# Kernel tuning notes

Hardware: AMD Instinct MI355X
Metric: run time of the kernel (lower is better)

The kernel has to match this reference:

```python
import jax, jax.numpy as jnp
import numpy as np

B, L, V, E, D, OUT = 64, 256, 50000, 512, 512, 3
PAD_IDX = 0
MAX_DIST = 11
NEG_INF = -1e9


def _mlp2(x, W1, b1, W2, b2):
    # Linear -> ReLU -> (Dropout=id) -> Linear -> ReLU -> (Dropout=id)
    h = jax.nn.relu(x @ W1 + b1)
    return jax.nn.relu(h @ W2 + b2)


def _masked_softmax(x, mask):
    return jax.nn.softmax(jnp.where(mask, x, NEG_INF), axis=-1)


def _rel_bias(n, dist_W):
    pos = jnp.arange(n)
    idx = jnp.clip(pos[None, :] - pos[:, None], -MAX_DIST, MAX_DIST) + MAX_DIST
    return dist_W[idx, 0]  # [n, n]


def _self_branch(x, mask, dist_W, Ws1, bs1, Ws2, bs2):
    # DeepDotAttention(x, x): shared MLP then dot scores [B, L, L]
    q = _mlp2(x, Ws1, bs1, Ws2, bs2)
    scores = jnp.einsum('bqd,bkd->bqk', q, q)
    n = x.shape[1]
    scores = scores + _rel_bias(n, dist_W)[None]           # relative-distance bias
    scores = jnp.where(jnp.eye(n, dtype=bool)[None], -jnp.inf, scores)  # mask diagonal
    scores = jnp.where(mask[:, None, :], scores, 0.0)      # zero padded keys (pre-softmax, as original)
    att = _masked_softmax(scores, mask[:, None, :])
    ctx = jnp.einsum('bqk,bkd->bqd', att, x)
    return jnp.concatenate([x, ctx], axis=-1)               # [B, L, 2E]


def setup_inputs() -> dict:
    key = jax.random.key(0)
    ks = jax.random.split(key, 20)

    def xavier(k, shape):
        fan_in, fan_out = shape[0], shape[1]
        lim = float(np.sqrt(6.0 / (fan_in + fan_out)))
        return jax.random.uniform(k, shape, jnp.float32, -lim, lim)

    embed_W = jax.random.normal(ks[0], (V, E), jnp.float32) * 0.1
    embed_W = embed_W.at[PAD_IDX].set(0.0)  # padding_idx
    inp = {
        'prem_input': jax.random.randint(ks[1], (B, L), 0, V),
        'hypo_input': jax.random.randint(ks[2], (B, L), 0, V),
        'embed_W': embed_W,
        'dist_W': jax.random.normal(ks[3], (2 * MAX_DIST + 1, 1), jnp.float32),
        # self-attention MLP (inp=E)
        'Ws1': xavier(ks[4], (E, D)), 'bs1': jnp.zeros((D,), jnp.float32),
        'Ws2': xavier(ks[5], (D, D)), 'bs2': jnp.zeros((D,), jnp.float32),
        # inter-attention MLP (inp=2E)
        'Wa1': xavier(ks[6], (2 * E, D)), 'ba1': jnp.zeros((D,), jnp.float32),
        'Wa2': xavier(ks[7], (D, D)), 'ba2': jnp.zeros((D,), jnp.float32),
        # compare MLP (inp=4E)
        'Wc1': xavier(ks[8], (4 * E, D)), 'bc1': jnp.zeros((D,), jnp.float32),
        'Wc2': xavier(ks[9], (D, D)), 'bc2': jnp.zeros((D,), jnp.float32),
        # aggregate MLP (inp=2D)
        'Wg1': xavier(ks[10], (2 * D, D)), 'bg1': jnp.zeros((D,), jnp.float32),
        'Wg2': xavier(ks[11], (D, D)), 'bg2': jnp.zeros((D,), jnp.float32),
        # output (no bias)
        'Wo': xavier(ks[12], (D, OUT)),
    }
    return inp


def reference(prem_input, hypo_input, embed_W, dist_W,
              Ws1, bs1, Ws2, bs2, Wa1, ba1, Wa2, ba2,
              Wc1, bc1, Wc2, bc2, Wg1, bg1, Wg2, bg2, Wo):
    prem_mask = prem_input != PAD_IDX  # [B, Lp]
    hypo_mask = hypo_input != PAD_IDX  # [B, Lh]

    prem = embed_W[prem_input]  # [B, Lp, E]
    hypo = embed_W[hypo_input]  # [B, Lh, E]

    prem = _self_branch(prem, prem_mask, dist_W, Ws1, bs1, Ws2, bs2)  # [B, Lp, 2E]
    hypo = _self_branch(hypo, hypo_mask, dist_W, Ws1, bs1, Ws2, bs2)  # [B, Lh, 2E]

    # inter-sentence DeepDotAttention
    pq = _mlp2(prem, Wa1, ba1, Wa2, ba2)
    hk = _mlp2(hypo, Wa1, ba1, Wa2, ba2)
    z = jnp.einsum('bpd,bhd->bph', pq, hk)  # [B, Lp, Lh]

    prem2hypo = _masked_softmax(z, hypo_mask[:, None, :])
    hypo2prem = _masked_softmax(jnp.swapaxes(z, 1, 2), prem_mask[:, None, :])

    attended_hypo = jnp.einsum('bph,bhd->bpd', prem2hypo, hypo)
    attended_prem = jnp.einsum('bhp,bpd->bhd', hypo2prem, prem)

    prem_cmp = _mlp2(jnp.concatenate([prem, attended_hypo], -1), Wc1, bc1, Wc2, bc2)
    hypo_cmp = _mlp2(jnp.concatenate([hypo, attended_prem], -1), Wc1, bc1, Wc2, bc2)
    prem_cmp = (prem_cmp * prem_mask[..., None].astype(prem_cmp.dtype)).sum(axis=1)
    hypo_cmp = (hypo_cmp * hypo_mask[..., None].astype(hypo_cmp.dtype)).sum(axis=1)

    agg = _mlp2(jnp.concatenate([prem_cmp, hypo_cmp], -1), Wg1, bg1, Wg2, bg2)
    return agg @ Wo  # [B, OUT]
```

## Files before the change

### kernel.cpp

```cpp
#include <hip/hip_runtime.h>
#include <math.h>

#define BB   64
#define LL   256
#define EE   512
#define DD   512
#define BL   (BB * LL)
#define BL2  (2 * BL)
#define MAX_DIST 11

typedef __attribute__((ext_vector_type(8))) short bf16x8;
typedef __attribute__((ext_vector_type(8))) unsigned short u16x8;
typedef __attribute__((ext_vector_type(4))) float f32x4;

__device__ __forceinline__ float bf2f(unsigned short u) {
    union { unsigned int u; float f; } v; v.u = ((unsigned int)u) << 16; return v.f;
}
__device__ __forceinline__ unsigned short f2bf(float f) {
    union { float f; unsigned int u; } v; v.f = f;
    unsigned int r = v.u + 0x7FFF + ((v.u >> 16) & 1);
    return (unsigned short)(r >> 16);
}

#define GLOAD16(g, l)                                                          \
    __builtin_amdgcn_global_load_lds(                                          \
        (const __attribute__((address_space(1))) void*)(g),                    \
        (__attribute__((address_space(3))) void*)(l), 16, 0, 0)

template <bool OBF16, int BN>
__global__ __launch_bounds__(256, 2) void bgemm_kernel(
    const unsigned short* __restrict__ A0, int K0, int lda0, long long bsA0,
    const unsigned short* __restrict__ A1, int lda1, long long bsA1,
    const unsigned short* __restrict__ B, int ldb, long long bsB,
    const float* __restrict__ bias,
    void* __restrict__ Cv, int ldc, long long bsC,
    int K, int relu)
{
    constexpr int NI = BN / 32;
    __shared__ unsigned short smem[(128 + BN) * 64];
    unsigned short* As = smem;
    unsigned short* Bs = smem + 128 * 64;

    const int tid  = threadIdx.x;
    const int wave = tid >> 6;
    const int lane = tid & 63;
    const int quad = lane >> 4;
    const int l15  = lane & 15;
    const int wm   = (wave >> 1) * 64;
    const int wn   = (wave & 1) * (BN / 2);
    const int row0 = blockIdx.x * 128;
    const int col0 = blockIdx.y * BN;
    const int b    = blockIdx.z;

    const unsigned short* A0b = A0 + (long long)b * bsA0;
    const unsigned short* A1b = A1 ? (A1 + (long long)b * bsA1) : nullptr;
    const unsigned short* Bb  = B + (long long)b * bsB;

    f32x4 acc[4][NI];
#pragma unroll
    for (int i = 0; i < 4; ++i)
#pragma unroll
        for (int j = 0; j < NI; ++j)
            acc[i][j] = (f32x4){0.f, 0.f, 0.f, 0.f};

    for (int kk = 0; kk < K; kk += 64) {
        const unsigned short* Ap; int lda, kloc;
        if (kk < K0) { Ap = A0b; lda = lda0; kloc = kk; }
        else         { Ap = A1b; lda = lda1; kloc = kk - K0; }
#pragma unroll
        for (int it = 0; it < 4; ++it) {
            const int c   = it * 256 + tid;
            const int row = c >> 3;
            const int kch = (c & 7) ^ (row & 7);
            GLOAD16(Ap + (long long)(row0 + row) * lda + kloc + kch * 8,
                    (char*)As + c * 16);
        }
#pragma unroll
        for (int it = 0; it < BN / 32; ++it) {
            const int c   = it * 256 + tid;
            const int row = c >> 3;
            const int kch = (c & 7) ^ (row & 7);
            GLOAD16(Bb + (long long)(col0 + row) * ldb + kk + kch * 8,
                    (char*)Bs + c * 16);
        }
        __syncthreads();

#pragma unroll
        for (int s = 0; s < 2; ++s) {
            bf16x8 fa[4], fb[NI];
#pragma unroll
            for (int mi = 0; mi < 4; ++mi) {
                const int r = wm + mi * 16 + l15;
                const int slot = (s * 4 + quad) ^ (r & 7);
                fa[mi] = *(const bf16x8*)&As[(r * 8 + slot) * 8];
            }
#pragma unroll
            for (int ni = 0; ni < NI; ++ni) {
                const int r = wn + ni * 16 + l15;
                const int slot = (s * 4 + quad) ^ (r & 7);
                fb[ni] = *(const bf16x8*)&Bs[(r * 8 + slot) * 8];
            }
#pragma unroll
            for (int mi = 0; mi < 4; ++mi)
#pragma unroll
                for (int ni = 0; ni < NI; ++ni)
                    acc[mi][ni] = __builtin_amdgcn_mfma_f32_16x16x32_bf16(
                        fa[mi], fb[ni], acc[mi][ni], 0, 0, 0);
        }
        __syncthreads();
    }

    float bv[NI];
#pragma unroll
    for (int ni = 0; ni < NI; ++ni)
        bv[ni] = bias ? bias[col0 + wn + ni * 16 + l15] : 0.f;

    if (OBF16) {
        float* Ls = (float*)smem;
        constexpr int LSW = BN + 1;
        constexpr int CPR = BN / 8;
        unsigned short* Cb = (unsigned short*)Cv + (long long)b * bsC;
#pragma unroll
        for (int h = 0; h < 4; ++h) {
            if ((wave >> 1) == (h >> 1)) {
                const int mi0 = (h & 1) * 2;
#pragma unroll
                for (int mm = 0; mm < 2; ++mm) {
#pragma unroll
                    for (int ni = 0; ni < NI; ++ni) {
#pragma unroll
                        for (int r = 0; r < 4; ++r) {
                            float x = acc[mi0 + mm][ni][r] + bv[ni];
                            if (relu) x = fmaxf(x, 0.f);
                            Ls[(mm * 16 + quad * 4 + r) * LSW +
                               wn + ni * 16 + l15] = x;
                        }
                    }
                }
            }
            __syncthreads();
#pragma unroll
            for (int it = 0; it < BN / 64; ++it) {
                const int c  = it * 256 + tid;
                const int lr = c / CPR;
                const int cc = (c % CPR) * 8;
                const float* src = &Ls[lr * LSW + cc];
                u16x8 u;
#pragma unroll
                for (int j = 0; j < 8; ++j) u[j] = f2bf(src[j]);
                *(u16x8*)(Cb + (long long)(row0 + h * 32 + lr) * ldc +
                          col0 + cc) = u;
            }
            __syncthreads();
        }
    } else {
        float* Cb = (float*)Cv + (long long)b * bsC;
#pragma unroll
        for (int mi = 0; mi < 4; ++mi)
#pragma unroll
            for (int ni = 0; ni < NI; ++ni) {
                const int colb = col0 + wn + ni * 16 + l15;
#pragma unroll
                for (int r = 0; r < 4; ++r) {
                    const int row = row0 + wm + mi * 16 + quad * 4 + r;
                    float x = acc[mi][ni][r] + bv[ni];
                    if (relu) x = fmaxf(x, 0.f);
                    Cb[(long long)row * ldc + colb] = x;
                }
            }
    }
}

struct WC6 {
    const float* s[6];
    unsigned short* d[6];
    int K[6];
};
__global__ void wconv6_kernel(WC6 wc)
{
    const int z = blockIdx.z;
    const int K = wc.K[z];
    const int k0 = blockIdx.y * 32;
    if (k0 >= K) return;
    const float* src = wc.s[z];
    unsigned short* dst = wc.d[z];
    __shared__ float tile[32][33];
    const int n0 = blockIdx.x * 32;
#pragma unroll
    for (int i = 0; i < 4; ++i)
        tile[threadIdx.y + i * 8][threadIdx.x] =
            src[(long long)(k0 + threadIdx.y + i * 8) * 512 + n0 + threadIdx.x];
    __syncthreads();
#pragma unroll
    for (int i = 0; i < 4; ++i)
        dst[(long long)(n0 + threadIdx.y + i * 8) * K + k0 + threadIdx.x] =
            f2bf(tile[threadIdx.x][threadIdx.y + i * 8]);
}

__global__ void btrans_kernel(const unsigned short* __restrict__ src, int lds_,
                              unsigned short* __restrict__ dst, int C, int bxor)
{
    __shared__ unsigned short tile[32][33];
    const int bz = blockIdx.z;
    const int bs = bz ^ bxor;
    const int c0 = blockIdx.x * 32, l0 = blockIdx.y * 32;
    const unsigned short* s = src + (long long)bs * 256 * lds_;
    unsigned short* d = dst + (long long)bz * C * 256;
#pragma unroll
    for (int i = 0; i < 4; ++i)
        tile[threadIdx.y + i * 8][threadIdx.x] =
            s[(long long)(l0 + threadIdx.y + i * 8) * lds_ + c0 + threadIdx.x];
    __syncthreads();
#pragma unroll
    for (int i = 0; i < 4; ++i)
        d[(long long)(c0 + threadIdx.y + i * 8) * 256 + l0 + threadIdx.x] =
            tile[threadIdx.x][threadIdx.y + i * 8];
}

__global__ void embed_kernel(const int* __restrict__ prem_tok,
                             const int* __restrict__ hypo_tok,
                             const float* __restrict__ W,
                             unsigned short* __restrict__ cat,
                             float* __restrict__ mask)
{
    const int row = blockIdx.x;
    const int t   = threadIdx.x;
    const int tok = row < BL ? prem_tok[row] : hypo_tok[row - BL];
    if (t == 0) mask[row] = (tok != 0) ? 1.0f : 0.0f;
    float4 v = ((const float4*)(W + (long long)tok * EE))[t];
    ushort4 o;
    o.x = f2bf(v.x); o.y = f2bf(v.y); o.z = f2bf(v.z); o.w = f2bf(v.w);
    ((ushort4*)(cat + (long long)row * 1024))[t] = o;
}

__device__ __forceinline__ float block_max(float v, float* red, int tid)
{
    red[tid] = v; __syncthreads();
    for (int st = 128; st > 0; st >>= 1) {
        if (tid < st) red[tid] = fmaxf(red[tid], red[tid + st]);
        __syncthreads();
    }
    float r = red[0]; __syncthreads();
    return r;
}
__device__ __forceinline__ float block_sum(float v, float* red, int tid)
{
    red[tid] = v; __syncthreads();
    for (int st = 128; st > 0; st >>= 1) {
        if (tid < st) red[tid] += red[tid + st];
        __syncthreads();
    }
    float r = red[0]; __syncthreads();
    return r;
}

__global__ void self_softmax_kernel(const float* __restrict__ S,
                                    unsigned short* __restrict__ SP,
                                    const float* __restrict__ mask,
                                    const float* __restrict__ distW)
{
    __shared__ float red[256];
    const int q = blockIdx.x, b = blockIdx.y, j = threadIdx.x;
    float s = S[((long long)b * LL + q) * LL + j];
    int d = j - q;
    d = d > MAX_DIST ? MAX_DIST : (d < -MAX_DIST ? -MAX_DIST : d);
    s += distW[d + MAX_DIST];
    if (j == q) s = -INFINITY;
    if (mask[b * LL + j] == 0.0f) s = -1e9f;
    float mx = block_max(s, red, j);
    float e  = expf(s - mx);
    float sm = block_sum(e, red, j);
    SP[((long long)b * LL + q) * LL + j] = f2bf(e / sm);
}

__global__ void row_softmax_kernel(const float* __restrict__ Z,
                                   unsigned short* __restrict__ SP,
                                   const float* __restrict__ maskK)
{
    __shared__ float red[256];
    const int p = blockIdx.x, b = blockIdx.y, j = threadIdx.x;
    float s = Z[((long long)b * LL + p) * LL + j];
    if (maskK[b * LL + j] == 0.0f) s = -1e9f;
    float mx = block_max(s, red, j);
    float e  = expf(s - mx);
    float sm = block_sum(e, red, j);
    SP[((long long)b * LL + p) * LL + j] = f2bf(e / sm);
}

__global__ void col_softmax_kernel(const float* __restrict__ Z,
                                   unsigned short* __restrict__ SP,
                                   const float* __restrict__ maskQ)
{
    __shared__ float red[256];
    const int h = blockIdx.x, b = blockIdx.y, p = threadIdx.x;
    float s = Z[((long long)b * LL + p) * LL + h];
    if (maskQ[b * LL + p] == 0.0f) s = -1e9f;
    float mx = block_max(s, red, p);
    float e  = expf(s - mx);
    float sm = block_sum(e, red, p);
    SP[((long long)b * LL + h) * LL + p] = f2bf(e / sm);
}

__global__ void masked_reduce_kernel(const unsigned short* __restrict__ Q,
                                     const float* __restrict__ MASK,
                                     float* __restrict__ R32)
{
    const int side = blockIdx.x >> 1;
    const int c    = (blockIdx.x & 1) * 256 + threadIdx.x;
    const int b    = blockIdx.y;
    const unsigned short* xb = Q + ((long long)(side * BL + b * LL)) * DD + c;
    const float* mb = MASK + side * BL + b * LL;
    float a0 = 0.f, a1 = 0.f, a2 = 0.f, a3 = 0.f;
#pragma unroll 4
    for (int r = 0; r < 64; ++r) {
        a0 = fmaf(bf2f(xb[(r       ) * DD]), mb[r      ], a0);
        a1 = fmaf(bf2f(xb[(r +  64) * DD]), mb[r +  64], a1);
        a2 = fmaf(bf2f(xb[(r + 128) * DD]), mb[r + 128], a2);
        a3 = fmaf(bf2f(xb[(r + 192) * DD]), mb[r + 192], a3);
    }
    R32[b * 1024 + side * 512 + c] = (a0 + a1) + (a2 + a3);
}

__global__ __launch_bounds__(256) void mlp_par_kernel(
    const float* __restrict__ X, const float* __restrict__ W,
    const float* __restrict__ bias, float* __restrict__ Y, int Kin)
{
    __shared__ float red[4][64];
    const int b  = blockIdx.y;
    const int n  = blockIdx.x * 64 + (threadIdx.x & 63);
    const int ts = threadIdx.x >> 6;
    const int kc = Kin >> 2;
    const float* x = X + (long long)b * Kin + ts * kc;
    const float* w = W + (long long)(ts * kc) * 512 + n;
    float a0 = 0.f, a1 = 0.f;
#pragma unroll 8
    for (int k = 0; k < kc; k += 2) {
        a0 = fmaf(x[k],     w[(long long)k * 512],       a0);
        a1 = fmaf(x[k + 1], w[(long long)(k + 1) * 512], a1);
    }
    red[ts][threadIdx.x & 63] = a0 + a1;
    __syncthreads();
    if (ts == 0) {
        float v = red[0][threadIdx.x] + red[1][threadIdx.x] +
                  red[2][threadIdx.x] + red[3][threadIdx.x] + bias[n];
        Y[b * 512 + n] = fmaxf(v, 0.f);
    }
}

__global__ void out_kernel(const float* __restrict__ G,
                           const float* __restrict__ Wo,
                           float* __restrict__ out)
{
    const int wid  = blockIdx.x * 4 + (threadIdx.x >> 6);
    const int lane = threadIdx.x & 63;
    const int b = wid / 3, o = wid % 3;
    float acc = 0.f;
#pragma unroll
    for (int j = 0; j < 8; ++j) {
        int d = lane + j * 64;
        acc = fmaf(G[b * DD + d], Wo[d * 3 + o], acc);
    }
#pragma unroll
    for (int st = 32; st > 0; st >>= 1)
        acc += __shfl_down(acc, st, 64);
    if (lane == 0) out[wid] = acc;
}

static inline void bgemm(hipStream_t stream, bool obf16, int bn,
                         const unsigned short* A0, int K0, int lda0, long long bsA0,
                         const unsigned short* A1, int lda1, long long bsA1,
                         const unsigned short* B, int ldb, long long bsB,
                         const float* bias,
                         void* C, int ldc, long long bsC,
                         int M, int N, int K, bool relu, int batch)
{
    dim3 grid(M / 128, N / bn, batch);
    if (bn == 256) {
        if (obf16)
            bgemm_kernel<true, 256><<<grid, 256, 0, stream>>>(A0, K0, lda0, bsA0, A1, lda1, bsA1,
                                                              B, ldb, bsB, bias, C, ldc, bsC, K, relu);
        else
            bgemm_kernel<false, 256><<<grid, 256, 0, stream>>>(A0, K0, lda0, bsA0, A1, lda1, bsA1,
                                                               B, ldb, bsB, bias, C, ldc, bsC, K, relu);
    } else {
        if (obf16)
            bgemm_kernel<true, 128><<<grid, 256, 0, stream>>>(A0, K0, lda0, bsA0, A1, lda1, bsA1,
                                                              B, ldb, bsB, bias, C, ldc, bsC, K, relu);
        else
            bgemm_kernel<false, 128><<<grid, 256, 0, stream>>>(A0, K0, lda0, bsA0, A1, lda1, bsA1,
                                                               B, ldb, bsB, bias, C, ldc, bsC, K, relu);
    }
}

extern "C" void kernel_launch(void* const* d_in, const int* in_sizes, int n_in,
                              void* d_out, int out_size, void* d_ws, size_t ws_size,
                              hipStream_t stream)
{
    (void)in_sizes; (void)n_in; (void)out_size; (void)ws_size;

    const int*   prem_tok = (const int*)d_in[0];
    const int*   hypo_tok = (const int*)d_in[1];
    const float* embW = (const float*)d_in[2];
    const float* dW   = (const float*)d_in[3];
    const float* Ws1  = (const float*)d_in[4];
    const float* bs1  = (const float*)d_in[5];
    const float* Ws2  = (const float*)d_in[6];
    const float* bs2  = (const float*)d_in[7];
    const float* Wa1  = (const float*)d_in[8];
    const float* ba1  = (const float*)d_in[9];
    const float* Wa2  = (const float*)d_in[10];
    const float* ba2  = (const float*)d_in[11];
    const float* Wc1  = (const float*)d_in[12];
    const float* bc1  = (const float*)d_in[13];
    const float* Wc2  = (const float*)d_in[14];
    const float* bc2  = (const float*)d_in[15];
    const float* Wg1  = (const float*)d_in[16];
    const float* bg1  = (const float*)d_in[17];
    const float* Wg2  = (const float*)d_in[18];
    const float* bg2  = (const float*)d_in[19];
    const float* Wo   = (const float*)d_in[20];
    float* out = (float*)d_out;

    char* ws = (char*)d_ws;
    size_t off = 0;
    auto alloc = [&](size_t bytes) {
        char* p = ws + off; off += (bytes + 255) & ~(size_t)255; return p;
    };
    unsigned short* CAT  = (unsigned short*)alloc((size_t)BL2 * 1024 * 2);
    unsigned short* VTF  = (unsigned short*)alloc((size_t)128 * 1024 * 256 * 2);
    unsigned short* Hb   = (unsigned short*)alloc((size_t)BL2 * 512 * 2);
    unsigned short* Q    = (unsigned short*)alloc((size_t)BL2 * 512 * 2);
    unsigned short* ATT  = (unsigned short*)alloc((size_t)BL2 * 1024 * 2);
    float*          S    = (float*)alloc((size_t)128 * LL * LL * 4);
    unsigned short* SP   = (unsigned short*)alloc((size_t)128 * LL * LL * 2);
    float*          MASK = (float*)alloc((size_t)BL2 * 4);
    float*          R32  = (float*)alloc((size_t)BB * 1024 * 4);
    float*          H64  = (float*)alloc((size_t)BB * 512 * 4);
    float*          G    = (float*)alloc((size_t)BB * 512 * 4);
    unsigned short* WTs1 = (unsigned short*)alloc((size_t)512 * 512 * 2);
    unsigned short* WTs2 = (unsigned short*)alloc((size_t)512 * 512 * 2);
    unsigned short* WTa1 = (unsigned short*)alloc((size_t)1024 * 512 * 2);
    unsigned short* WTa2 = (unsigned short*)alloc((size_t)512 * 512 * 2);
    unsigned short* WTc1 = (unsigned short*)alloc((size_t)2048 * 512 * 2);
    unsigned short* WTc2 = (unsigned short*)alloc((size_t)512 * 512 * 2);

    const long long bsQ = (long long)LL * DD;
    const long long bsS = (long long)LL * LL;
    const long long bsC = (long long)LL * 1024;

    dim3 tb(32, 8);

    WC6 wc;
    wc.s[0] = Ws1; wc.d[0] = WTs1; wc.K[0] = 512;
    wc.s[1] = Ws2; wc.d[1] = WTs2; wc.K[1] = 512;
    wc.s[2] = Wa1; wc.d[2] = WTa1; wc.K[2] = 1024;
    wc.s[3] = Wa2; wc.d[3] = WTa2; wc.K[3] = 512;
    wc.s[4] = Wc1; wc.d[4] = WTc1; wc.K[4] = 2048;
    wc.s[5] = Wc2; wc.d[5] = WTc2; wc.K[5] = 512;
    wconv6_kernel<<<dim3(16, 64, 6), tb, 0, stream>>>(wc);

    embed_kernel<<<BL2, 128, 0, stream>>>(prem_tok, hypo_tok, embW, CAT, MASK);

    bgemm(stream, true, 256, CAT, 512, 1024, 0, nullptr, 0, 0,
          WTs1, 512, 0, bs1, Hb, 512, 0, BL2, 512, 512, true, 1);
    bgemm(stream, true, 256, Hb, 512, 512, 0, nullptr, 0, 0,
          WTs2, 512, 0, bs2, Q, 512, 0, BL2, 512, 512, true, 1);
    btrans_kernel<<<dim3(16, 8, 128), tb, 0, stream>>>(CAT, 1024, VTF, 512, 0);
    bgemm(stream, false, 128, Q, 512, 512, bsQ, nullptr, 0, 0,
          Q, 512, bsQ, nullptr, S, 256, bsS, 256, 256, 512, false, 128);
    self_softmax_kernel<<<dim3(LL, 128), 256, 0, stream>>>(S, SP, MASK, dW);
    bgemm(stream, true, 256, SP, 256, 256, bsS, nullptr, 0, 0,
          VTF, 256, (long long)512 * 256, nullptr,
          CAT + 512, 1024, bsC, 256, 512, 256, false, 128);

    btrans_kernel<<<dim3(32, 8, 128), tb, 0, stream>>>(CAT, 1024, VTF, 1024, 64);

    bgemm(stream, true, 256, CAT, 1024, 1024, 0, nullptr, 0, 0,
          WTa1, 1024, 0, ba1, Hb, 512, 0, BL2, 512, 1024, true, 1);
    bgemm(stream, true, 256, Hb, 512, 512, 0, nullptr, 0, 0,
          WTa2, 512, 0, ba2, Q, 512, 0, BL2, 512, 512, true, 1);
    bgemm(stream, false, 128, Q, 512, 512, bsQ, nullptr, 0, 0,
          Q + (long long)BL * 512, 512, bsQ, nullptr,
          S, 256, bsS, 256, 256, 512, false, 64);

    row_softmax_kernel<<<dim3(LL, 64), 256, 0, stream>>>(S, SP, MASK + BL);
    col_softmax_kernel<<<dim3(LL, 64), 256, 0, stream>>>(S, SP + 64 * bsS, MASK);
    bgemm(stream, true, 256, SP, 256, 256, bsS, nullptr, 0, 0,
          VTF, 256, (long long)1024 * 256, nullptr,
          ATT, 1024, bsC, 256, 1024, 256, false, 128);

    bgemm(stream, true, 256, CAT, 1024, 1024, 0, ATT, 1024, 0,
          WTc1, 2048, 0, bc1, Hb, 512, 0, BL2, 512, 2048, true, 1);
    bgemm(stream, true, 256, Hb, 512, 512, 0, nullptr, 0, 0,
          WTc2, 512, 0, bc2, Q, 512, 0, BL2, 512, 512, true, 1);

    masked_reduce_kernel<<<dim3(4, BB), 256, 0, stream>>>(Q, MASK, R32);

    mlp_par_kernel<<<dim3(8, BB), 256, 0, stream>>>(R32, Wg1, bg1, H64, 1024);
    mlp_par_kernel<<<dim3(8, BB), 256, 0, stream>>>(H64, Wg2, bg2, G, 512);
    out_kernel<<<48, 256, 0, stream>>>(G, Wo, out);
}
```

Before: 705.2 us.

## Fuse softmax into score GEMM epilogues and masked reduce into final GEMM

The score GEMMs now use full 256-wide tiles, so each block owns whole rows. Bias, diagonal and padding masks and a row softmax are applied in registers, and bf16 probabilities are written directly, which removes the fp32 score buffer and the separate softmax kernels. Inter-attention computes both directions in one batched launch by XOR-swapping the batch index for B and for the mask. The last compare GEMM fuses bias, ReLU and the masked row sum through atomics into R32, which needs a memset and drops the Q write and the reduce kernel. Atomic accumulation makes the float sum order nondeterministic.

Result: faster. 630.2 us (-10.6%).

```diff
diff --git a/kernel.cpp b/kernel.cpp
--- a/kernel.cpp
+++ b/kernel.cpp
@@ -27,16 +27,20 @@
         (const __attribute__((address_space(1))) void*)(g),                    \
         (__attribute__((address_space(3))) void*)(l), 16, 0, 0)
 
-template <bool OBF16, int BN>
+template <int MODE>
 __global__ __launch_bounds__(256, 2) void bgemm_kernel(
     const unsigned short* __restrict__ A0, int K0, int lda0, long long bsA0,
     const unsigned short* __restrict__ A1, int lda1, long long bsA1,
-    const unsigned short* __restrict__ B, int ldb, long long bsB,
+    const unsigned short* __restrict__ B, int ldb, long long bsB, int bxor,
     const float* __restrict__ bias,
     void* __restrict__ Cv, int ldc, long long bsC,
-    int K, int relu)
-{
-    constexpr int NI = BN / 32;
+    int K, int relu,
+    const float* __restrict__ smask, const float* __restrict__ distW,
+    int diag, int maskXor,
+    float* __restrict__ rout, const float* __restrict__ rmask)
+{
+    constexpr int BN = 256;
+    constexpr int NI = 8;
     __shared__ unsigned short smem[(128 + BN) * 64];
     unsigned short* As = smem;
     unsigned short* Bs = smem + 128 * 64;
@@ -47,14 +51,14 @@
     const int quad = lane >> 4;
     const int l15  = lane & 15;
     const int wm   = (wave >> 1) * 64;
-    const int wn   = (wave & 1) * (BN / 2);
+    const int wn   = (wave & 1) * 128;
     const int row0 = blockIdx.x * 128;
     const int col0 = blockIdx.y * BN;
     const int b    = blockIdx.z;
 
     const unsigned short* A0b = A0 + (long long)b * bsA0;
     const unsigned short* A1b = A1 ? (A1 + (long long)b * bsA1) : nullptr;
-    const unsigned short* Bb  = B + (long long)b * bsB;
+    const unsigned short* Bb  = B + (long long)(b ^ bxor) * bsB;
 
     f32x4 acc[4][NI];
 #pragma unroll
@@ -76,7 +80,7 @@
                     (char*)As + c * 16);
         }
 #pragma unroll
-        for (int it = 0; it < BN / 32; ++it) {
+        for (int it = 0; it < 8; ++it) {
             const int c   = it * 256 + tid;
             const int row = c >> 3;
             const int kch = (c & 7) ^ (row & 7);
@@ -110,15 +114,165 @@
         __syncthreads();
     }
 
+    if constexpr (MODE == 2) {
+        float bv[NI];
+#pragma unroll
+        for (int ni = 0; ni < NI; ++ni)
+            bv[ni] = bias[col0 + wn + ni * 16 + l15];
+        float mrow[4][4];
+#pragma unroll
+        for (int mi = 0; mi < 4; ++mi)
+#pragma unroll
+            for (int r = 0; r < 4; ++r)
+                mrow[mi][r] = rmask[row0 + wm + mi * 16 + quad * 4 + r];
+        float t[NI];
+#pragma unroll
+        for (int ni = 0; ni < NI; ++ni) t[ni] = 0.f;
+#pragma unroll
+        for (int mi = 0; mi < 4; ++mi)
+#pragma unroll
+            for (int ni = 0; ni < NI; ++ni)
+#pragma unroll
+                for (int r = 0; r < 4; ++r) {
+                    float x = fmaxf(acc[mi][ni][r] + bv[ni], 0.f);
+                    t[ni] = fmaf(x, mrow[mi][r], t[ni]);
+                }
+#pragma unroll
+        for (int ni = 0; ni < NI; ++ni) {
+            t[ni] += __shfl_xor(t[ni], 16, 64);
+            t[ni] += __shfl_xor(t[ni], 32, 64);
+        }
+        if (quad == 0) {
+            const int sb = row0 >> 8;
+            const int base = (sb & 63) * 1024 + (sb >> 6) * 512;
+#pragma unroll
+            for (int ni = 0; ni < NI; ++ni)
+                atomicAdd(rout + base + col0 + wn + ni * 16 + l15, t[ni]);
+        }
+        return;
+    }
+
     float bv[NI];
-#pragma unroll
-    for (int ni = 0; ni < NI; ++ni)
-        bv[ni] = bias ? bias[col0 + wn + ni * 16 + l15] : 0.f;
-
-    if (OBF16) {
+    if constexpr (MODE == 0) {
+#pragma unroll
+        for (int ni = 0; ni < NI; ++ni)
+            bv[ni] = bias ? bias[col0 + wn + ni * 16 + l15] : 0.f;
+    } else {
+#pragma unroll
+        for (int ni = 0; ni < NI; ++ni) bv[ni] = 0.f;
+    }
+
+    if constexpr (MODE == 1) {
+        __shared__ float red[4][64];
+        const int kb = b ^ maskXor;
+        float mk[NI];
+#pragma unroll
+        for (int ni = 0; ni < NI; ++ni)
+            mk[ni] = smask[kb * 256 + wn + ni * 16 + l15];
+        float rm[4][4];
+#pragma unroll
+        for (int mi = 0; mi < 4; ++mi)
+#pragma unroll
+            for (int r = 0; r < 4; ++r) rm[mi][r] = -INFINITY;
+#pragma unroll
+        for (int mi = 0; mi < 4; ++mi)
+#pragma unroll
+            for (int r = 0; r < 4; ++r) {
+                const int q = row0 + wm + mi * 16 + quad * 4 + r;
+#pragma unroll
+                for (int ni = 0; ni < NI; ++ni) {
+                    const int j = wn + ni * 16 + l15;
+                    float s = acc[mi][ni][r];
+                    if (distW) {
+                        int d = j - q;
+                        d = d > MAX_DIST ? MAX_DIST : (d < -MAX_DIST ? -MAX_DIST : d);
+                        s += distW[d + MAX_DIST];
+                    }
+                    if (diag && j == q) s = -INFINITY;
+                    if (mk[ni] == 0.f) s = -1e9f;
+                    acc[mi][ni][r] = s;
+                    rm[mi][r] = fmaxf(rm[mi][r], s);
+                }
+            }
+#pragma unroll
+        for (int mi = 0; mi < 4; ++mi)
+#pragma unroll
+            for (int r = 0; r < 4; ++r) {
+                float v = rm[mi][r];
+                v = fmaxf(v, __shfl_xor(v, 1, 64));
+                v = fmaxf(v, __shfl_xor(v, 2, 64));
+                v = fmaxf(v, __shfl_xor(v, 4, 64));
+                v = fmaxf(v, __shfl_xor(v, 8, 64));
+                rm[mi][r] = v;
+            }
+        if (l15 == 0) {
+#pragma unroll
+            for (int mi = 0; mi < 4; ++mi)
+#pragma unroll
+                for (int r = 0; r < 4; ++r)
+                    red[wave][mi * 16 + quad * 4 + r] = rm[mi][r];
+        }
+        __syncthreads();
+#pragma unroll
+        for (int mi = 0; mi < 4; ++mi)
+#pragma unroll
+            for (int r = 0; r < 4; ++r)
+                rm[mi][r] = fmaxf(rm[mi][r],
+                                  red[wave ^ 1][mi * 16 + quad * 4 + r]);
+        float rs[4][4];
+#pragma unroll
+        for (int mi = 0; mi < 4; ++mi)
+#pragma unroll
+            for (int r = 0; r < 4; ++r) rs[mi][r] = 0.f;
+#pragma unroll
+        for (int mi = 0; mi < 4; ++mi)
+#pragma unroll
+            for (int ni = 0; ni < NI; ++ni)
+#pragma unroll
+                for (int r = 0; r < 4; ++r) {
+                    float e = __expf(acc[mi][ni][r] - rm[mi][r]);
+                    acc[mi][ni][r] = e;
+                    rs[mi][r] += e;
+                }
+#pragma unroll
+        for (int mi = 0; mi < 4; ++mi)
+#pragma unroll
+            for (int r = 0; r < 4; ++r) {
+                float v = rs[mi][r];
+                v += __shfl_xor(v, 1, 64);
+                v += __shfl_xor(v, 2, 64);
+                v += __shfl_xor(v, 4, 64);
+                v += __shfl_xor(v, 8, 64);
+                rs[mi][r] = v;
+            }
+        __syncthreads();
+        if (l15 == 0) {
+#pragma unroll
+            for (int mi = 0; mi < 4; ++mi)
+#pragma unroll
+                for (int r = 0; r < 4; ++r)
+                    red[wave][mi * 16 + quad * 4 + r] = rs[mi][r];
+        }
+        __syncthreads();
+#pragma unroll
+        for (int mi = 0; mi < 4; ++mi)
+#pragma unroll
+            for (int r = 0; r < 4; ++r) {
+                float inv = 1.f / (rs[mi][r] +
+                                   red[wave ^ 1][mi * 16 + quad * 4 + r] -
+                                   rs[mi][r] * 0.f);
+                float tot = rs[mi][r] + red[wave ^ 1][mi * 16 + quad * 4 + r];
+                inv = 1.f / tot;
+#pragma unroll
+                for (int ni = 0; ni < NI; ++ni)
+                    acc[mi][ni][r] *= inv;
+            }
+        __syncthreads();
+    }
+
+    {
         float* Ls = (float*)smem;
-        constexpr int LSW = BN + 1;
-        constexpr int CPR = BN / 8;
+        constexpr int LSW = 257;
         unsigned short* Cb = (unsigned short*)Cv + (long long)b * bsC;
 #pragma unroll
         for (int h = 0; h < 4; ++h) {
@@ -131,7 +285,7 @@
 #pragma unroll
                         for (int r = 0; r < 4; ++r) {
                             float x = acc[mi0 + mm][ni][r] + bv[ni];
-                            if (relu) x = fmaxf(x, 0.f);
+                            if (MODE == 0 && relu) x = fmaxf(x, 0.f);
                             Ls[(mm * 16 + quad * 4 + r) * LSW +
                                wn + ni * 16 + l15] = x;
                         }
@@ -140,10 +294,10 @@
             }
             __syncthreads();
 #pragma unroll
-            for (int it = 0; it < BN / 64; ++it) {
+            for (int it = 0; it < 4; ++it) {
                 const int c  = it * 256 + tid;
-                const int lr = c / CPR;
-                const int cc = (c % CPR) * 8;
+                const int lr = c >> 5;
+                const int cc = (c & 31) * 8;
                 const float* src = &Ls[lr * LSW + cc];
                 u16x8 u;
 #pragma unroll
@@ -153,21 +307,6 @@
             }
             __syncthreads();
         }
-    } else {
-        float* Cb = (float*)Cv + (long long)b * bsC;
-#pragma unroll
-        for (int mi = 0; mi < 4; ++mi)
-#pragma unroll
-            for (int ni = 0; ni < NI; ++ni) {
-                const int colb = col0 + wn + ni * 16 + l15;
-#pragma unroll
-                for (int r = 0; r < 4; ++r) {
-                    const int row = row0 + wm + mi * 16 + quad * 4 + r;
-                    float x = acc[mi][ni][r] + bv[ni];
-                    if (relu) x = fmaxf(x, 0.f);
-                    Cb[(long long)row * ldc + colb] = x;
-                }
-            }
     }
 }
 
@@ -231,94 +370,6 @@
     ushort4 o;
     o.x = f2bf(v.x); o.y = f2bf(v.y); o.z = f2bf(v.z); o.w = f2bf(v.w);
     ((ushort4*)(cat + (long long)row * 1024))[t] = o;
-}
-
-__device__ __forceinline__ float block_max(float v, float* red, int tid)
-{
-    red[tid] = v; __syncthreads();
-    for (int st = 128; st > 0; st >>= 1) {
-        if (tid < st) red[tid] = fmaxf(red[tid], red[tid + st]);
-        __syncthreads();
-    }
-    float r = red[0]; __syncthreads();
-    return r;
-}
-__device__ __forceinline__ float block_sum(float v, float* red, int tid)
-{
-    red[tid] = v; __syncthreads();
-    for (int st = 128; st > 0; st >>= 1) {
-        if (tid < st) red[tid] += red[tid + st];
-        __syncthreads();
-    }
-    float r = red[0]; __syncthreads();
-    return r;
-}
-
-__global__ void self_softmax_kernel(const float* __restrict__ S,
-                                    unsigned short* __restrict__ SP,
-                                    const float* __restrict__ mask,
-                                    const float* __restrict__ distW)
-{
-    __shared__ float red[256];
-    const int q = blockIdx.x, b = blockIdx.y, j = threadIdx.x;
-    float s = S[((long long)b * LL + q) * LL + j];
-    int d = j - q;
-    d = d > MAX_DIST ? MAX_DIST : (d < -MAX_DIST ? -MAX_DIST : d);
-    s += distW[d + MAX_DIST];
-    if (j == q) s = -INFINITY;
-    if (mask[b * LL + j] == 0.0f) s = -1e9f;
-    float mx = block_max(s, red, j);
-    float e  = expf(s - mx);
-    float sm = block_sum(e, red, j);
-    SP[((long long)b * LL + q) * LL + j] = f2bf(e / sm);
-}
-
-__global__ void row_softmax_kernel(const float* __restrict__ Z,
-                                   unsigned short* __restrict__ SP,
-                                   const float* __restrict__ maskK)
-{
-    __shared__ float red[256];
-    const int p = blockIdx.x, b = blockIdx.y, j = threadIdx.x;
-    float s = Z[((long long)b * LL + p) * LL + j];
-    if (maskK[b * LL + j] == 0.0f) s = -1e9f;
-    float mx = block_max(s, red, j);
-    float e  = expf(s - mx);
-    float sm = block_sum(e, red, j);
-    SP[((long long)b * LL + p) * LL + j] = f2bf(e / sm);
-}
-
-__global__ void col_softmax_kernel(const float* __restrict__ Z,
-                                   unsigned short* __restrict__ SP,
-                                   const float* __restrict__ maskQ)
-{
-    __shared__ float red[256];
-    const int h = blockIdx.x, b = blockIdx.y, p = threadIdx.x;
-    float s = Z[((long long)b * LL + p) * LL + h];
-    if (maskQ[b * LL + p] == 0.0f) s = -1e9f;
-    float mx = block_max(s, red, p);
-    float e  = expf(s - mx);
-    float sm = block_sum(e, red, p);
-    SP[((long long)b * LL + h) * LL + p] = f2bf(e / sm);
-}
-
-__global__ void masked_reduce_kernel(const unsigned short* __restrict__ Q,
-                                     const float* __restrict__ MASK,
-                                     float* __restrict__ R32)
-{
-    const int side = blockIdx.x >> 1;
-    const int c    = (blockIdx.x & 1) * 256 + threadIdx.x;
-    const int b    = blockIdx.y;
-    const unsigned short* xb = Q + ((long long)(side * BL + b * LL)) * DD + c;
-    const float* mb = MASK + side * BL + b * LL;
-    float a0 = 0.f, a1 = 0.f, a2 = 0.f, a3 = 0.f;
-#pragma unroll 4
-    for (int r = 0; r < 64; ++r) {
-        a0 = fmaf(bf2f(xb[(r       ) * DD]), mb[r      ], a0);
-        a1 = fmaf(bf2f(xb[(r +  64) * DD]), mb[r +  64], a1);
-        a2 = fmaf(bf2f(xb[(r + 128) * DD]), mb[r + 128], a2);
-        a3 = fmaf(bf2f(xb[(r + 192) * DD]), mb[r + 192], a3);
-    }
-    R32[b * 1024 + side * 512 + c] = (a0 + a1) + (a2 + a3);
 }
 
 __global__ __launch_bounds__(256) void mlp_par_kernel(
@@ -366,30 +417,26 @@
     if (lane == 0) out[wid] = acc;
 }
 
-static inline void bgemm(hipStream_t stream, bool obf16, int bn,
-                         const unsigned short* A0, int K0, int lda0, long long bsA0,
-                         const unsigned short* A1, int lda1, long long bsA1,
-                         const unsigned short* B, int ldb, long long bsB,
-                         const float* bias,
-                         void* C, int ldc, long long bsC,
-                         int M, int N, int K, bool relu, int batch)
-{
-    dim3 grid(M / 128, N / bn, batch);
-    if (bn == 256) {
-        if (obf16)
-            bgemm_kernel<true, 256><<<grid, 256, 0, stream>>>(A0, K0, lda0, bsA0, A1, lda1, bsA1,
-                                                              B, ldb, bsB, bias, C, ldc, bsC, K, relu);
-        else
-            bgemm_kernel<false, 256><<<grid, 256, 0, stream>>>(A0, K0, lda0, bsA0, A1, lda1, bsA1,
-                                                               B, ldb, bsB, bias, C, ldc, bsC, K, relu);
-    } else {
-        if (obf16)
-            bgemm_kernel<true, 128><<<grid, 256, 0, stream>>>(A0, K0, lda0, bsA0, A1, lda1, bsA1,
-                                                              B, ldb, bsB, bias, C, ldc, bsC, K, relu);
-        else
-            bgemm_kernel<false, 128><<<grid, 256, 0, stream>>>(A0, K0, lda0, bsA0, A1, lda1, bsA1,
-                                                               B, ldb, bsB, bias, C, ldc, bsC, K, relu);
-    }
+struct GemmArgs {
+    const unsigned short *A0, *A1, *B;
+    int K0, lda0, lda1, ldb;
+    long long bsA0, bsA1, bsB;
+    int bxor;
+    const float* bias;
+    void* C; int ldc; long long bsC;
+    int M, N, K, relu, batch;
+    const float* smask; const float* distW; int diag; int maskXor;
+    float* rout; const float* rmask;
+};
+
+template <int MODE>
+static inline void bgemm_launch(hipStream_t stream, const GemmArgs& a)
+{
+    dim3 grid(a.M / 128, a.N / 256, a.batch);
+    bgemm_kernel<MODE><<<grid, 256, 0, stream>>>(
+        a.A0, a.K0, a.lda0, a.bsA0, a.A1, a.lda1, a.bsA1,
+        a.B, a.ldb, a.bsB, a.bxor, a.bias, a.C, a.ldc, a.bsC,
+        a.K, a.relu, a.smask, a.distW, a.diag, a.maskXor, a.rout, a.rmask);
 }
 
 extern "C" void kernel_launch(void* const* d_in, const int* in_sizes, int n_in,
@@ -431,7 +478,6 @@
     unsigned short* Hb   = (unsigned short*)alloc((size_t)BL2 * 512 * 2);
     unsigned short* Q    = (unsigned short*)alloc((size_t)BL2 * 512 * 2);
     unsigned short* ATT  = (unsigned short*)alloc((size_t)BL2 * 1024 * 2);
-    float*          S    = (float*)alloc((size_t)128 * LL * LL * 4);
     unsigned short* SP   = (unsigned short*)alloc((size_t)128 * LL * LL * 2);
     float*          MASK = (float*)alloc((size_t)BL2 * 4);
     float*          R32  = (float*)alloc((size_t)BB * 1024 * 4);
@@ -458,43 +504,69 @@
     wc.s[4] = Wc1; wc.d[4] = WTc1; wc.K[4] = 2048;
     wc.s[5] = Wc2; wc.d[5] = WTc2; wc.K[5] = 512;
     wconv6_kernel<<<dim3(16, 64, 6), tb, 0, stream>>>(wc);
+    hipMemsetAsync(R32, 0, (size_t)BB * 1024 * 4, stream);
 
     embed_kernel<<<BL2, 128, 0, stream>>>(prem_tok, hypo_tok, embW, CAT, MASK);
 
-    bgemm(stream, true, 256, CAT, 512, 1024, 0, nullptr, 0, 0,
-          WTs1, 512, 0, bs1, Hb, 512, 0, BL2, 512, 512, true, 1);
-    bgemm(stream, true, 256, Hb, 512, 512, 0, nullptr, 0, 0,
-          WTs2, 512, 0, bs2, Q, 512, 0, BL2, 512, 512, true, 1);
+    GemmArgs a = {};
+
+    a = {}; a.A0 = CAT; a.K0 = 512; a.lda0 = 1024; a.B = WTs1; a.ldb = 512;
+    a.bias = bs1; a.C = Hb; a.ldc = 512; a.M = BL2; a.N = 512; a.K = 512;
+    a.relu = 1; a.batch = 1;
+    bgemm_launch<0>(stream, a);
+    a = {}; a.A0 = Hb; a.K0 = 512; a.lda0 = 512; a.B = WTs2; a.ldb = 512;
+    a.bias = bs2; a.C = Q; a.ldc = 512; a.M = BL2; a.N = 512; a.K = 512;
+    a.relu = 1; a.batch = 1;
+    bgemm_launch<0>(stream, a);
+
     btrans_kernel<<<dim3(16, 8, 128), tb, 0, stream>>>(CAT, 1024, VTF, 512, 0);
-    bgemm(stream, false, 128, Q, 512, 512, bsQ, nullptr, 0, 0,
-          Q, 512, bsQ, nullptr, S, 256, bsS, 256, 256, 512, false, 128);
-    self_softmax_kernel<<<dim3(LL, 128), 256, 0, stream>>>(S, SP, MASK, dW);
-    bgemm(stream, true, 256, SP, 256, 256, bsS, nullptr, 0, 0,
-          VTF, 256, (long long)512 * 256, nullptr,
-          CAT + 512, 1024, bsC, 256, 512, 256, false, 128);
+
+    a = {}; a.A0 = Q; a.K0 = 512; a.lda0 = 512; a.bsA0 = bsQ;
+    a.B = Q; a.ldb = 512; a.bsB = bsQ; a.bxor = 0;
+    a.C = SP; a.ldc = 256; a.bsC = bsS; a.M = 256; a.N = 256; a.K = 512;
+    a.batch = 128; a.smask = MASK; a.distW = dW; a.diag = 1; a.maskXor = 0;
+    bgemm_launch<1>(stream, a);
+
+    a = {}; a.A0 = SP; a.K0 = 256; a.lda0 = 256; a.bsA0 = bsS;
+    a.B = VTF; a.ldb = 256; a.bsB = (long long)512 * 256;
+    a.C = CAT + 512; a.ldc = 1024; a.bsC = bsC;
+    a.M = 256; a.N = 512; a.K = 256; a.batch = 128;
+    bgemm_launch<0>(stream, a);
 
     btrans_kernel<<<dim3(32, 8, 128), tb, 0, stream>>>(CAT, 1024, VTF, 1024, 64);
 
-    bgemm(stream, true, 256, CAT, 1024, 1024, 0, nullptr, 0, 0,
-          WTa1, 1024, 0, ba1, Hb, 512, 0, BL2, 512, 1024, true, 1);
-    bgemm(stream, true, 256, Hb, 512, 512, 0, nullptr, 0, 0,
-          WTa2, 512, 0, ba2, Q, 512, 0, BL2, 512, 512, true, 1);
-    bgemm(stream, false, 128, Q, 512, 512, bsQ, nullptr, 0, 0,
-          Q + (long long)BL * 512, 512, bsQ, nullptr,
-          S, 256, bsS, 256, 256, 512, false, 64);
-
-    row_softmax_kernel<<<dim3(LL, 64), 256, 0, stream>>>(S, SP, MASK + BL);
-    col_softmax_kernel<<<dim3(LL, 64), 256, 0, stream>>>(S, SP + 64 * bsS, MASK);
-    bgemm(stream, true, 256, SP, 256, 256, bsS, nullptr, 0, 0,
-          VTF, 256, (long long)1024 * 256, nullptr,
-          ATT, 1024, bsC, 256, 1024, 256, false, 128);
-
-    bgemm(stream, true, 256, CAT, 1024, 1024, 0, ATT, 1024, 0,
-          WTc1, 2048, 0, bc1, Hb, 512, 0, BL2, 512, 2048, true, 1);
-    bgemm(stream, true, 256, Hb, 512, 512, 0, nullptr, 0, 0,
-          WTc2, 512, 0, bc2, Q, 512, 0, BL2, 512, 512, true, 1);
-
-    masked_reduce_kernel<<<dim3(4, BB), 256, 0, stream>>>(Q, MASK, R32);
+    a = {}; a.A0 = CAT; a.K0 = 1024; a.lda0 = 1024; a.B = WTa1; a.ldb = 1024;
+    a.bias = ba1; a.C = Hb; a.ldc = 512; a.M = BL2; a.N = 512; a.K = 1024;
+    a.relu = 1; a.batch = 1;
+    bgemm_launch<0>(stream, a);
+    a = {}; a.A0 = Hb; a.K0 = 512; a.lda0 = 512; a.B = WTa2; a.ldb = 512;
+    a.bias = ba2; a.C = Q; a.ldc = 512; a.M = BL2; a.N = 512; a.K = 512;
+    a.relu = 1; a.batch = 1;
+    bgemm_launch<0>(stream, a);
+
+    a = {}; a.A0 = Q; a.K0 = 512; a.lda0 = 512; a.bsA0 = bsQ;
+    a.B = Q; a.ldb = 512; a.bsB = bsQ; a.bxor = 64;
+    a.C = SP; a.ldc = 256; a.bsC = bsS; a.M = 256; a.N = 256; a.K = 512;
+    a.batch = 128; a.smask = MASK; a.distW = nullptr; a.diag = 0; a.maskXor = 64;
+    bgemm_launch<1>(stream, a);
+
+    a = {}; a.A0 = SP; a.K0 = 256; a.lda0 = 256; a.bsA0 = bsS;
+    a.B = VTF; a.ldb = 256; a.bsB = (long long)1024 * 256;
+    a.C = ATT; a.ldc = 1024; a.bsC = bsC;
+    a.M = 256; a.N = 1024; a.K = 256; a.batch = 128;
+    bgemm_launch<0>(stream, a);
+
+    a = {}; a.A0 = CAT; a.K0 = 1024; a.lda0 = 1024;
+    a.A1 = ATT; a.lda1 = 1024;
+    a.B = WTc1; a.ldb = 2048; a.bias = bc1;
+    a.C = Hb; a.ldc = 512; a.M = BL2; a.N = 512; a.K = 2048;
+    a.relu = 1; a.batch = 1;
+    bgemm_launch<0>(stream, a);
+
+    a = {}; a.A0 = Hb; a.K0 = 512; a.lda0 = 512; a.B = WTc2; a.ldb = 512;
+    a.bias = bc2; a.M = BL2; a.N = 512; a.K = 512; a.relu = 1; a.batch = 1;
+    a.rout = R32; a.rmask = MASK; a.C = Hb;
+    bgemm_launch<2>(stream, a);
 
     mlp_par_kernel<<<dim3(8, BB), 256, 0, stream>>>(R32, Wg1, bg1, H64, 1024);
     mlp_par_kernel<<<dim3(8, BB), 256, 0, stream>>>(H64, Wg2, bg2, G, 512);
```
